# Performance work log

Hardware: AMD Instinct MI355X
Metric: run time of the kernel (lower is better)

Reference implementation:

```python
import jax, jax.numpy as jnp
import numpy as np

NUM_HEADS = 8  # init kwarg num_heads


def setup_inputs() -> dict:
    key = jax.random.key(0)
    ks = jax.random.split(key, 6)
    B, H, W, C, ws = 16, 128, 128, 256, 8
    hd = C // NUM_HEADS
    s = 0.02
    return {
        "x": jax.random.normal(ks[0], (B, H * W, C), jnp.float32),
        "qkv_w": jax.random.normal(ks[1], (3 * C, C), jnp.float32) * s,
        "qkv_b": jnp.zeros((3 * C,), jnp.float32),
        "proj_w": jax.random.normal(ks[2], (C, C), jnp.float32) * s,
        "proj_b": jnp.zeros((C,), jnp.float32),
        "rel_pos_h": jax.random.normal(ks[3], (2 * ws - 1, hd), jnp.float32) * s,
        "rel_pos_w": jax.random.normal(ks[4], (2 * ws - 1, hd), jnp.float32) * s,
        "H": 128,
        "W": 128,
    }


def reference(x, qkv_w, qkv_b, proj_w, proj_b, rel_pos_h, rel_pos_w, H, W):
    # WindowAttention forward (H, W divisible by window -> pad is a no-op).
    ws = (rel_pos_h.shape[0] + 1) // 2          # window size (8)
    B, N, C = x.shape
    heads = NUM_HEADS
    hd = C // heads
    scale = hd ** -0.5

    # window_partition: (B, H, W, C) -> (B*nWh*nWw, ws*ws, C)
    xw = x.reshape(B, H // ws, ws, W // ws, ws, C)
    xw = xw.transpose(0, 1, 3, 2, 4, 5).reshape(-1, ws * ws, C)
    Bw, Nw, _ = xw.shape

    qkv = xw @ qkv_w.T + qkv_b                   # (Bw, Nw, 3C)
    qkv = qkv.reshape(Bw, Nw, 3, heads, hd).transpose(2, 0, 3, 1, 4)
    q, k, v = qkv[0], qkv[1], qkv[2]             # (Bw, heads, Nw, hd)

    attn = jnp.einsum('bhqd,bhkd->bhqk', q * scale, k)

    # gather-based spatial relative position bias (calc_rel_pos_spatial, q==k shape)
    idx = jnp.arange(ws)[:, None] - jnp.arange(ws)[None, :] + (ws - 1)  # (ws, ws)
    Rh = rel_pos_h[idx]                          # (ws, ws, hd)
    Rw = rel_pos_w[idx]                          # (ws, ws, hd)
    r_q = q.reshape(Bw, heads, ws, ws, hd)
    rel_h = jnp.einsum('byhwc,hkc->byhwk', r_q, Rh)   # (Bw, heads, ws, ws, ws)
    rel_w_ = jnp.einsum('byhwc,wkc->byhwk', r_q, Rw)  # (Bw, heads, ws, ws, ws)
    attn = (attn.reshape(Bw, heads, ws, ws, ws, ws)
            + rel_h[:, :, :, :, :, None]
            + rel_w_[:, :, :, :, None, :]).reshape(Bw, heads, Nw, Nw)

    attn = jax.nn.softmax(attn, axis=-1)
    attn = jnp.where(jnp.isinf(attn) | jnp.isnan(attn), 0.0, attn)

    out = jnp.einsum('bhqk,bhkd->bhqd', attn, v)
    out = out.transpose(0, 2, 1, 3).reshape(Bw, Nw, C)
    out = out @ proj_w.T + proj_b

    # window_reverse: (Bw, Nw, C) -> (B, H, W, C) -> (B, N, C)
    out = out.reshape(B, H // ws, W // ws, ws, ws, C)
    out = out.transpose(0, 1, 3, 2, 4, 5).reshape(B, H, W, C)
    return out.reshape(B, N, C)
```

## Files before the change

### kernel.cpp

```cpp
#include <hip/hip_runtime.h>
#include <hip/hip_bf16.h>
#include <cstdint>
#include <cstddef>

typedef __bf16 bft;
typedef __bf16 bf16x8 __attribute__((ext_vector_type(8)));
typedef __bf16 bf16x4 __attribute__((ext_vector_type(4)));
typedef float  f32x4  __attribute__((ext_vector_type(4)));

#define MFMA(a, b, c) __builtin_amdgcn_mfma_f32_16x16x32_bf16(a, b, c, 0, 0, 0)

constexpr float SCALE = 0.17677669529663689f;
constexpr float INVS  = 5.656854249492381f;

__global__ __launch_bounds__(256) void cvt_kernel(const float* __restrict__ s,
                                                  bft* __restrict__ d, int n) {
  int stride = gridDim.x * blockDim.x;
  for (int i = blockIdx.x * blockDim.x + threadIdx.x; i * 4 < n; i += stride) {
    const float4 v = *reinterpret_cast<const float4*>(s + (size_t)i * 4);
    bf16x4 o = {(bft)v.x, (bft)v.y, (bft)v.z, (bft)v.w};
    *reinterpret_cast<bf16x4*>(d + (size_t)i * 4) = o;
  }
}

__global__ __launch_bounds__(256, 1) void win_fused(
    const float* __restrict__ X, const bft* __restrict__ Wq,
    const float* __restrict__ Bq, const bft* __restrict__ Wp,
    const float* __restrict__ Bp, const float* __restrict__ rph,
    const float* __restrict__ rpw, float* __restrict__ Out) {
  __shared__ bft QK[36864];
  __shared__ bft Vv[17408];

  const int t = threadIdx.x, lane = t & 63, wv = t >> 6;
  const int l15 = lane & 15, l4 = lane >> 4;
  const int win = blockIdx.x;
  const int b = win >> 8, wh = (win >> 4) & 15, ww = win & 15;

  bf16x8 rhf = {}, rwf = {};
  if (l15 < 15) {
    const float* th = rph + l15 * 32 + l4 * 8;
    const float* tw = rpw + l15 * 32 + l4 * 8;
#pragma unroll
    for (int j = 0; j < 8; ++j) {
      rhf[j] = (bft)(th[j] * INVS);
      rwf[j] = (bft)(tw[j] * INVS);
    }
  }

  {
    const float* xw =
        X + ((size_t)b * 16384 + (size_t)(wh * 8) * 128 + ww * 8) * 256;
#pragma unroll
    for (int yy = 0; yy < 2; ++yy) {
      const int y = wv * 2 + yy;
      const float* src = xw + (size_t)y * 32768;
#pragma unroll
      for (int it = 0; it < 8; ++it) {
        float4 v = *reinterpret_cast<const float4*>(src + (it * 64 + lane) * 4);
        bf16x4 o = {(bft)v.x, (bft)v.y, (bft)v.z, (bft)v.w};
        *reinterpret_cast<bf16x4*>(&QK[(y * 8 + it) * 272 + lane * 4]) = o;
      }
    }
  }
  __syncthreads();

  bf16x8 af[4][8];
#pragma unroll
  for (int m = 0; m < 4; ++m)
#pragma unroll
    for (int kk = 0; kk < 8; ++kk)
      af[m][kk] = *reinterpret_cast<const bf16x8*>(
          &QK[(m * 16 + l15) * 272 + kk * 32 + l4 * 8]);
  __syncthreads();

#pragma unroll
  for (int hh = 0; hh < 2; ++hh) {
    const int h = wv + hh * 4;
#pragma unroll
    for (int comp = 0; comp < 3; ++comp) {
#pragma unroll
      for (int half = 0; half < 2; ++half) {
        const int n0 = comp * 256 + h * 32 + half * 16;
        bf16x8 bw[8];
#pragma unroll
        for (int kk = 0; kk < 8; ++kk)
          bw[kk] = *reinterpret_cast<const bf16x8*>(
              &Wq[(size_t)(n0 + l15) * 256 + kk * 32 + l4 * 8]);
        f32x4 acc[4] = {};
#pragma unroll
        for (int kk = 0; kk < 8; ++kk)
#pragma unroll
          for (int m = 0; m < 4; ++m) acc[m] = MFMA(af[m][kk], bw[kk], acc[m]);
        const float bias = Bq[n0 + l15];
        if (comp == 0) {
#pragma unroll
          for (int m = 0; m < 4; ++m)
#pragma unroll
            for (int r = 0; r < 4; ++r)
              QK[h * 4608 + (m * 16 + l4 * 4 + r) * 36 + half * 16 + l15] =
                  (bft)((acc[m][r] + bias) * SCALE);
        } else if (comp == 1) {
#pragma unroll
          for (int m = 0; m < 4; ++m)
#pragma unroll
            for (int r = 0; r < 4; ++r)
              QK[h * 4608 + 2304 + (m * 16 + l4 * 4 + r) * 36 + half * 16 +
                 l15] = (bft)(acc[m][r] + bias);
        } else {
#pragma unroll
          for (int m = 0; m < 4; ++m) {
            bf16x4 pk = {(bft)(acc[m][0] + bias), (bft)(acc[m][1] + bias),
                         (bft)(acc[m][2] + bias), (bft)(acc[m][3] + bias)};
            *reinterpret_cast<bf16x4*>(
                &Vv[h * 2176 + (half * 16 + l15) * 68 + m * 16 + l4 * 4]) = pk;
          }
        }
      }
    }
  }
  __syncthreads();

#pragma unroll
  for (int hh = 0; hh < 2; ++hh) {
    const int h = wv + hh * 4;
    const int qb = h * 4608, kb = qb + 2304, vb = h * 2176;
    bf16x8 qf[4], kf[4];
#pragma unroll
    for (int i = 0; i < 4; ++i) {
      bf16x4 lo, hi;
      lo = *reinterpret_cast<const bf16x4*>(&QK[qb + (i * 16 + l15) * 36 + l4 * 8]);
      hi = *reinterpret_cast<const bf16x4*>(&QK[qb + (i * 16 + l15) * 36 + l4 * 8 + 4]);
      qf[i] = __builtin_shufflevector(lo, hi, 0, 1, 2, 3, 4, 5, 6, 7);
      lo = *reinterpret_cast<const bf16x4*>(&QK[kb + (i * 16 + l15) * 36 + l4 * 8]);
      hi = *reinterpret_cast<const bf16x4*>(&QK[kb + (i * 16 + l15) * 36 + l4 * 8 + 4]);
      kf[i] = __builtin_shufflevector(lo, hi, 0, 1, 2, 3, 4, 5, 6, 7);
    }
    f32x4 s[4][4], gh[4], gw[4];
#pragma unroll
    for (int i = 0; i < 4; ++i) {
      f32x4 z = {};
      gh[i] = MFMA(qf[i], rhf, z);
      gw[i] = MFMA(qf[i], rwf, z);
#pragma unroll
      for (int j = 0; j < 4; ++j) {
        f32x4 z2 = {};
        s[i][j] = MFMA(qf[i], kf[j], z2);
      }
    }
#pragma unroll
    for (int i = 0; i < 4; ++i)
#pragma unroll
      for (int r = 0; r < 4; ++r) {
        const int row = i * 16 + l4 * 4 + r;
        const int qy = row >> 3, qx = row & 7;
        const float bwv =
            __shfl(gw[i][r], (lane & 48) + (qx + 7 - (l15 & 7)));
        float v0[4], mx = -3.0e38f;
#pragma unroll
        for (int j = 0; j < 4; ++j) {
          const float bh =
              __shfl(gh[i][r], (lane & 48) + (qy + 7 - (j * 2 + (l15 >> 3))));
          v0[j] = s[i][j][r] + bh + bwv;
          mx = fmaxf(mx, v0[j]);
        }
        mx = fmaxf(mx, __shfl_xor(mx, 1));
        mx = fmaxf(mx, __shfl_xor(mx, 2));
        mx = fmaxf(mx, __shfl_xor(mx, 4));
        mx = fmaxf(mx, __shfl_xor(mx, 8));
        float sum = 0.f;
#pragma unroll
        for (int j = 0; j < 4; ++j) {
          v0[j] = __expf(v0[j] - mx);
          sum += v0[j];
        }
        sum += __shfl_xor(sum, 1);
        sum += __shfl_xor(sum, 2);
        sum += __shfl_xor(sum, 4);
        sum += __shfl_xor(sum, 8);
        const float inv = 1.0f / sum;
#pragma unroll
        for (int j = 0; j < 4; ++j)
          QK[qb + row * 68 + j * 16 + l15] = (bft)(v0[j] * inv);
      }
    __syncthreads();
    bf16x8 pf[4][2], vf[2][2];
#pragma unroll
    for (int i = 0; i < 4; ++i)
#pragma unroll
      for (int kc = 0; kc < 2; ++kc) {
        bf16x4 lo = *reinterpret_cast<const bf16x4*>(
            &QK[qb + (i * 16 + l15) * 68 + kc * 32 + l4 * 8]);
        bf16x4 hi = *reinterpret_cast<const bf16x4*>(
            &QK[qb + (i * 16 + l15) * 68 + kc * 32 + l4 * 8 + 4]);
        pf[i][kc] = __builtin_shufflevector(lo, hi, 0, 1, 2, 3, 4, 5, 6, 7);
      }
#pragma unroll
    for (int j2 = 0; j2 < 2; ++j2)
#pragma unroll
      for (int kc = 0; kc < 2; ++kc) {
        bf16x4 lo = *reinterpret_cast<const bf16x4*>(
            &Vv[vb + (j2 * 16 + l15) * 68 + kc * 32 + l4 * 8]);
        bf16x4 hi = *reinterpret_cast<const bf16x4*>(
            &Vv[vb + (j2 * 16 + l15) * 68 + kc * 32 + l4 * 8 + 4]);
        vf[j2][kc] = __builtin_shufflevector(lo, hi, 0, 1, 2, 3, 4, 5, 6, 7);
      }
    f32x4 o[4][2] = {};
#pragma unroll
    for (int i = 0; i < 4; ++i)
#pragma unroll
      for (int j2 = 0; j2 < 2; ++j2) {
        o[i][j2] = MFMA(pf[i][0], vf[j2][0], o[i][j2]);
        o[i][j2] = MFMA(pf[i][1], vf[j2][1], o[i][j2]);
      }
    __syncthreads();
#pragma unroll
    for (int i = 0; i < 4; ++i)
#pragma unroll
      for (int j2 = 0; j2 < 2; ++j2)
#pragma unroll
        for (int r = 0; r < 4; ++r)
          QK[qb + (i * 16 + l4 * 4 + r) * 36 + j2 * 16 + l15] =
              (bft)o[i][j2][r];
  }
  __syncthreads();

  float pbias[4];
#pragma unroll
  for (int n = 0; n < 4; ++n) pbias[n] = Bp[wv * 64 + n * 16 + l15];
  f32x4 po[4][4] = {};
#pragma unroll
  for (int sH = 0; sH < 8; ++sH) {
    bf16x8 oa[4];
#pragma unroll
    for (int m = 0; m < 4; ++m) {
      bf16x4 lo = *reinterpret_cast<const bf16x4*>(
          &QK[sH * 4608 + (m * 16 + l15) * 36 + l4 * 8]);
      bf16x4 hi = *reinterpret_cast<const bf16x4*>(
          &QK[sH * 4608 + (m * 16 + l15) * 36 + l4 * 8 + 4]);
      oa[m] = __builtin_shufflevector(lo, hi, 0, 1, 2, 3, 4, 5, 6, 7);
    }
#pragma unroll
    for (int n = 0; n < 4; ++n) {
      bf16x8 wb = *reinterpret_cast<const bf16x8*>(
          &Wp[(size_t)(wv * 64 + n * 16 + l15) * 256 + sH * 32 + l4 * 8]);
#pragma unroll
      for (int m = 0; m < 4; ++m) po[m][n] = MFMA(oa[m], wb, po[m][n]);
    }
  }
  float* ob = Out + ((size_t)b * 16384 + (size_t)(wh * 8) * 128 + ww * 8) * 256;
#pragma unroll
  for (int m = 0; m < 4; ++m)
#pragma unroll
    for (int r = 0; r < 4; ++r) {
      const int tok = m * 16 + l4 * 4 + r;
      float* og = ob + ((size_t)(tok >> 3) * 128 + (tok & 7)) * 256;
#pragma unroll
      for (int n = 0; n < 4; ++n)
        og[wv * 64 + n * 16 + l15] = po[m][n][r] + pbias[n];
    }
}

extern "C" void kernel_launch(void* const* d_in, const int* in_sizes, int n_in,
                              void* d_out, int out_size, void* d_ws,
                              size_t ws_size, hipStream_t stream) {
  const float* x      = (const float*)d_in[0];
  const float* qkv_w  = (const float*)d_in[1];
  const float* qkv_b  = (const float*)d_in[2];
  const float* proj_w = (const float*)d_in[3];
  const float* proj_b = (const float*)d_in[4];
  const float* rph    = (const float*)d_in[5];
  const float* rpw    = (const float*)d_in[6];
  float* out = (float*)d_out;

  if (ws_size < 524288) return;
  bft* qw = (bft*)d_ws;
  bft* pw = (bft*)((char*)d_ws + 393216);

  cvt_kernel<<<192, 256, 0, stream>>>(qkv_w, qw, 196608);
  cvt_kernel<<<64, 256, 0, stream>>>(proj_w, pw, 65536);
  win_fused<<<4096, 256, 0, stream>>>(x, qw, qkv_b, pw, proj_b, rph, rpw, out);
}
```

Measured before the change: 913.6 us.

## Cut LDS footprint to fit two blocks per CU by per-wave head scratch

Each wave now processes its heads one at a time in a private Q/K scratch region, so shared memory drops from about 108KB to about 77KB and launch bounds request two blocks per CU. The X tile is no longer staged through LDS; each wave loads its A fragments directly from global memory, converting fp32 to bf16, and reloads them for its second head. Per-head attention outputs go to a separate padded buffer so that the intermediate block barriers can be removed, and the projection stage reads full 16-byte fragments. The trade-off is duplicated global reads of X and register pressure under the tighter occupancy bound.

```diff
diff --git a/kernel.cpp b/kernel.cpp
--- a/kernel.cpp
+++ b/kernel.cpp
@@ -23,18 +23,20 @@
   }
 }
 
-__global__ __launch_bounds__(256, 1) void win_fused(
+__global__ __launch_bounds__(256, 2) void win_fused(
     const float* __restrict__ X, const bft* __restrict__ Wq,
     const float* __restrict__ Bq, const bft* __restrict__ Wp,
     const float* __restrict__ Bp, const float* __restrict__ rph,
     const float* __restrict__ rpw, float* __restrict__ Out) {
-  __shared__ bft QK[36864];
-  __shared__ bft Vv[17408];
+  __shared__ alignas(16) bft QK[18432];
+  __shared__ alignas(16) bft VO[20480];
 
   const int t = threadIdx.x, lane = t & 63, wv = t >> 6;
   const int l15 = lane & 15, l4 = lane >> 4;
   const int win = blockIdx.x;
   const int b = win >> 8, wh = (win >> 4) & 15, ww = win & 15;
+  const float* xw =
+      X + ((size_t)b * 16384 + (size_t)(wh * 8) * 128 + ww * 8) * 256;
 
   bf16x8 rhf = {}, rwf = {};
   if (l15 < 15) {
@@ -47,35 +49,29 @@
     }
   }
 
-  {
-    const float* xw =
-        X + ((size_t)b * 16384 + (size_t)(wh * 8) * 128 + ww * 8) * 256;
-#pragma unroll
-    for (int yy = 0; yy < 2; ++yy) {
-      const int y = wv * 2 + yy;
-      const float* src = xw + (size_t)y * 32768;
-#pragma unroll
-      for (int it = 0; it < 8; ++it) {
-        float4 v = *reinterpret_cast<const float4*>(src + (it * 64 + lane) * 4);
-        bf16x4 o = {(bft)v.x, (bft)v.y, (bft)v.z, (bft)v.w};
-        *reinterpret_cast<bf16x4*>(&QK[(y * 8 + it) * 272 + lane * 4]) = o;
-      }
-    }
-  }
-  __syncthreads();
-
-  bf16x8 af[4][8];
-#pragma unroll
-  for (int m = 0; m < 4; ++m)
-#pragma unroll
-    for (int kk = 0; kk < 8; ++kk)
-      af[m][kk] = *reinterpret_cast<const bf16x8*>(
-          &QK[(m * 16 + l15) * 272 + kk * 32 + l4 * 8]);
-  __syncthreads();
-
-#pragma unroll
-  for (int hh = 0; hh < 2; ++hh) {
-    const int h = wv + hh * 4;
+  const int qb = wv * 4608, kb = qb + 2304;
+
+#pragma unroll 1
+  for (int p = 0; p < 2; ++p) {
+    const int h = wv + p * 4;
+    const int vb = h * 2560;
+
+    bf16x8 af[4][8];
+#pragma unroll
+    for (int m = 0; m < 4; ++m) {
+      const int tok = m * 16 + l15;
+      const float* rowp = xw + (size_t)((tok >> 3) * 128 + (tok & 7)) * 256;
+#pragma unroll
+      for (int kk = 0; kk < 8; ++kk) {
+        const float* cp = rowp + kk * 32 + l4 * 8;
+        float4 a = *reinterpret_cast<const float4*>(cp);
+        float4 c2 = *reinterpret_cast<const float4*>(cp + 4);
+        bf16x8 f = {(bft)a.x, (bft)a.y, (bft)a.z, (bft)a.w,
+                    (bft)c2.x, (bft)c2.y, (bft)c2.z, (bft)c2.w};
+        af[m][kk] = f;
+      }
+    }
+
 #pragma unroll
     for (int comp = 0; comp < 3; ++comp) {
 #pragma unroll
@@ -97,33 +93,27 @@
           for (int m = 0; m < 4; ++m)
 #pragma unroll
             for (int r = 0; r < 4; ++r)
-              QK[h * 4608 + (m * 16 + l4 * 4 + r) * 36 + half * 16 + l15] =
+              QK[qb + (m * 16 + l4 * 4 + r) * 36 + half * 16 + l15] =
                   (bft)((acc[m][r] + bias) * SCALE);
         } else if (comp == 1) {
 #pragma unroll
           for (int m = 0; m < 4; ++m)
 #pragma unroll
             for (int r = 0; r < 4; ++r)
-              QK[h * 4608 + 2304 + (m * 16 + l4 * 4 + r) * 36 + half * 16 +
-                 l15] = (bft)(acc[m][r] + bias);
+              QK[kb + (m * 16 + l4 * 4 + r) * 36 + half * 16 + l15] =
+                  (bft)(acc[m][r] + bias);
         } else {
 #pragma unroll
           for (int m = 0; m < 4; ++m) {
             bf16x4 pk = {(bft)(acc[m][0] + bias), (bft)(acc[m][1] + bias),
                          (bft)(acc[m][2] + bias), (bft)(acc[m][3] + bias)};
             *reinterpret_cast<bf16x4*>(
-                &Vv[h * 2176 + (half * 16 + l15) * 68 + m * 16 + l4 * 4]) = pk;
+                &VO[vb + (half * 16 + l15) * 68 + m * 16 + l4 * 4]) = pk;
           }
         }
       }
     }
-  }
-  __syncthreads();
-
-#pragma unroll
-  for (int hh = 0; hh < 2; ++hh) {
-    const int h = wv + hh * 4;
-    const int qb = h * 4608, kb = qb + 2304, vb = h * 2176;
+
     bf16x8 qf[4], kf[4];
 #pragma unroll
     for (int i = 0; i < 4; ++i) {
@@ -153,8 +143,7 @@
       for (int r = 0; r < 4; ++r) {
         const int row = i * 16 + l4 * 4 + r;
         const int qy = row >> 3, qx = row & 7;
-        const float bwv =
-            __shfl(gw[i][r], (lane & 48) + (qx + 7 - (l15 & 7)));
+        const float bwv = __shfl(gw[i][r], (lane & 48) + (qx + 7 - (l15 & 7)));
         float v0[4], mx = -3.0e38f;
 #pragma unroll
         for (int j = 0; j < 4; ++j) {
@@ -182,7 +171,6 @@
         for (int j = 0; j < 4; ++j)
           QK[qb + row * 68 + j * 16 + l15] = (bft)(v0[j] * inv);
       }
-    __syncthreads();
     bf16x8 pf[4][2], vf[2][2];
 #pragma unroll
     for (int i = 0; i < 4; ++i)
@@ -199,9 +187,9 @@
 #pragma unroll
       for (int kc = 0; kc < 2; ++kc) {
         bf16x4 lo = *reinterpret_cast<const bf16x4*>(
-            &Vv[vb + (j2 * 16 + l15) * 68 + kc * 32 + l4 * 8]);
+            &VO[vb + (j2 * 16 + l15) * 68 + kc * 32 + l4 * 8]);
         bf16x4 hi = *reinterpret_cast<const bf16x4*>(
-            &Vv[vb + (j2 * 16 + l15) * 68 + kc * 32 + l4 * 8 + 4]);
+            &VO[vb + (j2 * 16 + l15) * 68 + kc * 32 + l4 * 8 + 4]);
         vf[j2][kc] = __builtin_shufflevector(lo, hi, 0, 1, 2, 3, 4, 5, 6, 7);
       }
     f32x4 o[4][2] = {};
@@ -212,33 +200,25 @@
         o[i][j2] = MFMA(pf[i][0], vf[j2][0], o[i][j2]);
         o[i][j2] = MFMA(pf[i][1], vf[j2][1], o[i][j2]);
       }
-    __syncthreads();
 #pragma unroll
     for (int i = 0; i < 4; ++i)
 #pragma unroll
       for (int j2 = 0; j2 < 2; ++j2)
 #pragma unroll
         for (int r = 0; r < 4; ++r)
-          QK[qb + (i * 16 + l4 * 4 + r) * 36 + j2 * 16 + l15] =
+          VO[vb + (i * 16 + l4 * 4 + r) * 40 + j2 * 16 + l15] =
               (bft)o[i][j2][r];
   }
   __syncthreads();
 
-  float pbias[4];
-#pragma unroll
-  for (int n = 0; n < 4; ++n) pbias[n] = Bp[wv * 64 + n * 16 + l15];
   f32x4 po[4][4] = {};
 #pragma unroll
   for (int sH = 0; sH < 8; ++sH) {
     bf16x8 oa[4];
 #pragma unroll
-    for (int m = 0; m < 4; ++m) {
-      bf16x4 lo = *reinterpret_cast<const bf16x4*>(
-          &QK[sH * 4608 + (m * 16 + l15) * 36 + l4 * 8]);
-      bf16x4 hi = *reinterpret_cast<const bf16x4*>(
-          &QK[sH * 4608 + (m * 16 + l15) * 36 + l4 * 8 + 4]);
-      oa[m] = __builtin_shufflevector(lo, hi, 0, 1, 2, 3, 4, 5, 6, 7);
-    }
+    for (int m = 0; m < 4; ++m)
+      oa[m] = *reinterpret_cast<const bf16x8*>(
+          &VO[sH * 2560 + (m * 16 + l15) * 40 + l4 * 8]);
 #pragma unroll
     for (int n = 0; n < 4; ++n) {
       bf16x8 wb = *reinterpret_cast<const bf16x8*>(
@@ -247,6 +227,9 @@
       for (int m = 0; m < 4; ++m) po[m][n] = MFMA(oa[m], wb, po[m][n]);
     }
   }
+  float pbias[4];
+#pragma unroll
+  for (int n = 0; n < 4; ++n) pbias[n] = Bp[wv * 64 + n * 16 + l15];
   float* ob = Out + ((size_t)b * 16384 + (size_t)(wh * 8) * 128 + ww * 8) * 256;
 #pragma unroll
   for (int m = 0; m < 4; ++m)
```

Result: faster. 875.1 us (-4.2%).
